# Kernel optimization log

Hardware: AMD Instinct MI355X
Metric: run time of the kernel (lower is better)

Reference implementation:

```python
import jax, jax.numpy as jnp
import numpy as np

B, S, D, H = 4, 2048, 2048, 16
DK = D // H  # 128
EPS = 1e-6


def setup_inputs() -> dict:
    key = jax.random.key(0)
    ks = jax.random.split(key, 8)
    scale = 1.0 / np.sqrt(D)
    return {
        "q": jax.random.normal(ks[0], (B, S, D), jnp.float32),
        "k": jax.random.normal(ks[1], (B, S, D), jnp.float32),
        "v": jax.random.normal(ks[2], (B, S, D), jnp.float32),
        "Wq": jax.random.normal(ks[3], (D, D), jnp.float32) * scale,
        "Wk": jax.random.normal(ks[4], (D, D), jnp.float32) * scale,
        "Wv": jax.random.normal(ks[5], (D, D), jnp.float32) * scale,
        "Wo": jax.random.normal(ks[6], (D, D), jnp.float32) * scale,
        "gamma": jnp.ones((D,), jnp.float32),
        "beta": jnp.zeros((D,), jnp.float32),
    }


def reference(q, k, v, Wq, Wk, Wv, Wo, gamma, beta):
    residual = q
    # projections (Linear with weight (out,in): x @ W^T)
    Q = (q @ Wq.T).reshape(B, S, H, DK)
    K = (k @ Wk.T).reshape(B, S, H, DK)
    V = (v @ Wv.T).reshape(B, S, H, DK)
    # faithful to source: permute(2,0,1,3) then flatten -> head-major (H*B, S, DK)
    Q = jnp.transpose(Q, (2, 0, 1, 3)).reshape(H * B, S, DK)
    K = jnp.transpose(K, (2, 0, 1, 3)).reshape(H * B, S, DK)
    V = jnp.transpose(V, (2, 0, 1, 3)).reshape(H * B, S, DK)
    scores = jnp.einsum("nqd,nkd->nqk", Q, K) / jnp.sqrt(jnp.float32(DK))
    attn = jax.nn.softmax(scores, axis=-1)  # (H*B, S, S)
    context = jnp.einsum("nqk,nkd->nqd", attn, V)
    # faithful to source: view (H*B,S,DK) as (B,H,S,DK) (batch-major reinterpretation)
    context = context.reshape(B, H, S, DK)
    context = jnp.transpose(context, (0, 2, 1, 3)).reshape(B, S, H * DK)
    output = context @ Wo.T  # dropout=0.0 (eval)
    output = output + residual
    mean = jnp.mean(output, axis=-1, keepdims=True)
    var = jnp.mean(jnp.square(output - mean), axis=-1, keepdims=True)
    output = (output - mean) / jnp.sqrt(var + EPS) * gamma + beta
    return output, attn
```

## Files before the change

kernel.cpp:

```cpp
#include <hip/hip_runtime.h>
#include <cstdint>

typedef __attribute__((ext_vector_type(8))) short short8;
typedef __attribute__((ext_vector_type(4))) float f32x4;
typedef __attribute__((ext_vector_type(2))) unsigned u32x2;
typedef unsigned short ushort_t;

constexpr int Bc = 4, Sc = 2048, Dc = 2048, Hc = 16, DKc = 128;
constexpr long NTOK = (long)Bc * Sc;
constexpr long OUT_ELEMS = NTOK * (long)Dc;
constexpr float SCALE = 0.08838834764831843f;

__device__ __forceinline__ ushort_t f2bf(float f) {
  unsigned u = __builtin_bit_cast(unsigned, f);
  u = (u + 0x7FFFu + ((u >> 16) & 1u)) >> 16;
  return (ushort_t)u;
}

__device__ __forceinline__ short8 pack8(const f32x4& a, const f32x4& b) {
  short8 h;
  h[0] = (short)f2bf(a[0]); h[1] = (short)f2bf(a[1]);
  h[2] = (short)f2bf(a[2]); h[3] = (short)f2bf(a[3]);
  h[4] = (short)f2bf(b[0]); h[5] = (short)f2bf(b[1]);
  h[6] = (short)f2bf(b[2]); h[7] = (short)f2bf(b[3]);
  return h;
}

__device__ __forceinline__ void gl2lds16(const ushort_t* g, ushort_t* l) {
  __builtin_amdgcn_global_load_lds(
      (__attribute__((address_space(1))) unsigned int*)(g),
      (__attribute__((address_space(3))) unsigned int*)(l), 16, 0, 0);
}

__device__ __forceinline__ void bar() {
  asm volatile("" ::: "memory");
  __builtin_amdgcn_s_barrier();
  asm volatile("" ::: "memory");
}

__global__ __launch_bounds__(512, 2)
void proj_gemm(const float* __restrict__ qf, const float* __restrict__ kf,
               const float* __restrict__ vf,
               const ushort_t* __restrict__ Wqb, const ushort_t* __restrict__ Wkb,
               const ushort_t* __restrict__ Wvb,
               ushort_t* __restrict__ Qb, ushort_t* __restrict__ Kb,
               ushort_t* __restrict__ VTo)
{
  __shared__ __align__(16) ushort_t SM[2][2][2][128 * 64];

  const int z = blockIdx.z;
  const float* Afull = (z == 0) ? qf : (z == 1) ? kf : vf;
  const ushort_t* Bp = (z == 0) ? Wqb : (z == 1) ? Wkb : Wvb;
  ushort_t* Cp = (z == 0) ? Qb : (z == 1) ? Kb : VTo;

  const int tid = threadIdx.x, lane = tid & 63, wave = tid >> 6;
  const int wm = wave >> 2, wn = wave & 3;

  const int lin = blockIdx.y * 8 + blockIdx.x;
  const int swz = (lin & 7) * 32 + (lin >> 3);
  const long n0 = (long)(swz & 7) * 256;
  const long m0 = (long)(swz >> 3) * 256;

  constexpr int NT = 32;

  const float*    Ag = Afull + m0 * (long)Dc;
  const ushort_t* Bg = Bp + n0 * (long)Dc;

  auto stageB = [&](ushort_t* dst, int kt, int ht) {
#pragma unroll
    for (int c = 0; c < 2; ++c) {
      int U = (c * 8 + wave) * 64 + lane;
      int row = U >> 3, p = U & 7, u = p ^ (row & 7);
      gl2lds16(Bg + (long)(ht * 128 + row) * Dc + kt * 64 + u * 8,
               dst + (c * 8 + wave) * 512);
    }
  };
  auto loadA = [&](int kt, f32x4 alo[2][2], f32x4 ahi[2][2]) {
#pragma unroll
    for (int ht = 0; ht < 2; ++ht)
#pragma unroll
      for (int c = 0; c < 2; ++c) {
        int U = (c * 8 + wave) * 64 + lane;
        int row = U >> 3, p = U & 7, u = p ^ (row & 7);
        const float* g = Ag + (long)(ht * 128 + row) * Dc + kt * 64 + u * 8;
        alo[ht][c] = *(const f32x4*)g;
        ahi[ht][c] = *(const f32x4*)(g + 4);
      }
  };
  auto writeA = [&](int buf, const f32x4 alo[2][2], const f32x4 ahi[2][2]) {
#pragma unroll
    for (int ht = 0; ht < 2; ++ht)
#pragma unroll
      for (int c = 0; c < 2; ++c) {
        int chunk = c * 8 + wave;
        *(short8*)(&SM[0][buf][ht][chunk * 512 + lane * 8]) =
            pack8(alo[ht][c], ahi[ht][c]);
      }
  };

  stageB(&SM[1][0][0][0], 0, 0);
  stageB(&SM[1][0][1][0], 0, 1);
  stageB(&SM[1][1][0][0], 1, 0);
  {
    f32x4 alo[2][2], ahi[2][2];
    loadA(0, alo, ahi);
    asm volatile("s_waitcnt vmcnt(0)" ::: "memory");
    writeA(0, alo, ahi);
    asm volatile("s_waitcnt lgkmcnt(0)" ::: "memory");
  }
  __builtin_amdgcn_s_barrier();
  asm volatile("" ::: "memory");

  f32x4 acc[8][4] = {};

  for (int kt = 0; kt < NT; ++kt) {
    const int cur = kt & 1;
    const ushort_t* Acur = &SM[0][cur][0][0];
    const ushort_t* Bcur = &SM[1][cur][0][0];
    const int k1 = (kt + 1) & (NT - 1);
    const int k2 = (kt + 2) & (NT - 1);
    short8 af[4][2], bq0[2][2], bq1[2][2];
    f32x4 alo[2][2], ahi[2][2];

#pragma unroll
    for (int mf = 0; mf < 4; ++mf)
#pragma unroll
      for (int ks = 0; ks < 2; ++ks) {
        int r = mf * 16 + (lane & 15);
        int u = ks * 4 + (lane >> 4), p = u ^ (r & 7);
        af[mf][ks] = *(const short8*)(Acur + wm * (128 * 64) + r * 64 + p * 8);
      }
#pragma unroll
    for (int nf = 0; nf < 2; ++nf)
#pragma unroll
      for (int ks = 0; ks < 2; ++ks) {
        int r = (wn & 1) * 64 + nf * 16 + (lane & 15);
        int u = ks * 4 + (lane >> 4), p = u ^ (r & 7);
        bq0[nf][ks] = *(const short8*)(Bcur + (wn >> 1) * (128 * 64) + r * 64 + p * 8);
      }
    stageB(&SM[1][cur ^ 1][1][0], k1, 1);
    bar();
    __builtin_amdgcn_s_setprio(1);
#pragma unroll
    for (int mf = 0; mf < 4; ++mf)
#pragma unroll
      for (int nf = 0; nf < 2; ++nf)
#pragma unroll
        for (int ks = 0; ks < 2; ++ks)
          acc[mf][nf] = __builtin_amdgcn_mfma_f32_16x16x32_bf16(af[mf][ks], bq0[nf][ks], acc[mf][nf], 0, 0, 0);
    __builtin_amdgcn_s_setprio(0);
    bar();

#pragma unroll
    for (int nf = 0; nf < 2; ++nf)
#pragma unroll
      for (int ks = 0; ks < 2; ++ks) {
        int r = (wn & 1) * 64 + 32 + nf * 16 + (lane & 15);
        int u = ks * 4 + (lane >> 4), p = u ^ (r & 7);
        bq1[nf][ks] = *(const short8*)(Bcur + (wn >> 1) * (128 * 64) + r * 64 + p * 8);
      }
    loadA(k1, alo, ahi);
    bar();
    __builtin_amdgcn_s_setprio(1);
#pragma unroll
    for (int mf = 0; mf < 4; ++mf)
#pragma unroll
      for (int nf = 0; nf < 2; ++nf)
#pragma unroll
        for (int ks = 0; ks < 2; ++ks)
          acc[mf][2 + nf] = __builtin_amdgcn_mfma_f32_16x16x32_bf16(af[mf][ks], bq1[nf][ks], acc[mf][2 + nf], 0, 0, 0);
    __builtin_amdgcn_s_setprio(0);
    bar();

#pragma unroll
    for (int mf = 0; mf < 4; ++mf)
#pragma unroll
      for (int ks = 0; ks < 2; ++ks) {
        int r = 64 + mf * 16 + (lane & 15);
        int u = ks * 4 + (lane >> 4), p = u ^ (r & 7);
        af[mf][ks] = *(const short8*)(Acur + wm * (128 * 64) + r * 64 + p * 8);
      }
    stageB(&SM[1][cur][0][0], k2, 0);
    bar();
    __builtin_amdgcn_s_setprio(1);
#pragma unroll
    for (int mf = 0; mf < 4; ++mf)
#pragma unroll
      for (int nf = 0; nf < 2; ++nf)
#pragma unroll
        for (int ks = 0; ks < 2; ++ks)
          acc[4 + mf][nf] = __builtin_amdgcn_mfma_f32_16x16x32_bf16(af[mf][ks], bq0[nf][ks], acc[4 + mf][nf], 0, 0, 0);
    __builtin_amdgcn_s_setprio(0);
    bar();

    asm volatile("s_waitcnt vmcnt(2)" ::: "memory");
    writeA(cur ^ 1, alo, ahi);
    asm volatile("s_waitcnt lgkmcnt(0)" ::: "memory");
    bar();
    __builtin_amdgcn_s_setprio(1);
#pragma unroll
    for (int mf = 0; mf < 4; ++mf)
#pragma unroll
      for (int nf = 0; nf < 2; ++nf)
#pragma unroll
        for (int ks = 0; ks < 2; ++ks)
          acc[4 + mf][2 + nf] = __builtin_amdgcn_mfma_f32_16x16x32_bf16(af[mf][ks], bq1[nf][ks], acc[4 + mf][2 + nf], 0, 0, 0);
    __builtin_amdgcn_s_setprio(0);
    bar();
  }

  asm volatile("s_waitcnt vmcnt(0)" ::: "memory");

  if (z == 2) {
    bar();
    char* Tb = (char*)&SM[0][0][0][0];
#pragma unroll
    for (int mq = 0; mq < 8; ++mq) {
#pragma unroll
      for (int nq = 0; nq < 4; ++nq) {
        int rg = wm * 128 + (mq >> 2) * 64 + (mq & 3) * 16 + ((lane >> 4) * 4);
        int cg = wn * 64 + (nq >> 1) * 32 + (nq & 1) * 16 + (lane & 15);
        u32x2 t;
        t[0] = (unsigned)f2bf(acc[mq][nq][0]) | ((unsigned)f2bf(acc[mq][nq][1]) << 16);
        t[1] = (unsigned)f2bf(acc[mq][nq][2]) | ((unsigned)f2bf(acc[mq][nq][3]) << 16);
        int off = cg * 512 + (((rg >> 3) ^ (cg & 31)) * 16) + (rg & 7) * 2;
        *(u32x2*)(Tb + off) = t;
      }
    }
    bar();
    const long bq = m0 >> 11;
    const long s0 = m0 & 2047;
#pragma unroll
    for (int i = 0; i < 16; ++i) {
      int row = i * 16 + (tid >> 5);
      int un  = tid & 31;
      int p = un ^ (row & 31);
      short8 val = *(const short8*)(Tb + row * 512 + p * 16);
      long cgg = n0 + row;
      long vtrow = ((cgg >> 7) * 4 + bq) * 128 + (cgg & 127);
      *(short8*)(&Cp[vtrow * (long)Sc + s0 + un * 8]) = val;
    }
  } else {
#pragma unroll
    for (int mq = 0; mq < 8; ++mq) {
#pragma unroll
      for (int nq = 0; nq < 4; ++nq) {
#pragma unroll
        for (int j = 0; j < 4; ++j) {
          long rg = m0 + wm * 128 + (mq >> 2) * 64 + (mq & 3) * 16 + ((lane >> 4) * 4) + j;
          long cg = n0 + wn * 64 + (nq >> 1) * 32 + (nq & 1) * 16 + (lane & 15);
          Cp[rg * (long)Dc + cg] = f2bf(acc[mq][nq][j]);
        }
      }
    }
  }
}

__global__ __launch_bounds__(512, 2)
void out_gemm(const ushort_t* __restrict__ Ap, const ushort_t* __restrict__ Bp,
              float* __restrict__ Cp, const float* __restrict__ residual)
{
  __shared__ __align__(16) ushort_t SM[2][2][2][128 * 64];

  const int tid = threadIdx.x, lane = tid & 63, wave = tid >> 6;
  const int wm = wave >> 2, wn = wave & 3;
  const int lin = blockIdx.y * 8 + blockIdx.x;
  const int swz = (lin & 7) * 32 + (lin >> 3);
  const long n0 = (long)(swz & 7) * 256;
  const long m0 = (long)(swz >> 3) * 256;
  constexpr int NT = 32;

  const ushort_t* Ag = Ap + m0 * (long)Dc;
  const ushort_t* Bg = Bp + n0 * (long)Dc;

  auto stage = [&](const ushort_t* gb, ushort_t* dst, int kt, int ht) {
#pragma unroll
    for (int c = 0; c < 2; ++c) {
      int U = (c * 8 + wave) * 64 + lane;
      int row = U >> 3, p = U & 7, u = p ^ (row & 7);
      gl2lds16(gb + (long)(ht * 128 + row) * Dc + kt * 64 + u * 8,
               dst + (c * 8 + wave) * 512);
    }
  };

  stage(Bg, &SM[1][0][0][0], 0, 0);
  stage(Ag, &SM[0][0][0][0], 0, 0);
  stage(Bg, &SM[1][0][1][0], 0, 1);
  stage(Ag, &SM[0][0][1][0], 0, 1);
  stage(Bg, &SM[1][1][0][0], 1, 0);
  stage(Ag, &SM[0][1][0][0], 1, 0);
  asm volatile("s_waitcnt vmcnt(4)" ::: "memory");
  __builtin_amdgcn_s_barrier();
  asm volatile("" ::: "memory");

  f32x4 acc[8][4] = {};

  for (int kt = 0; kt < NT; ++kt) {
    const int cur = kt & 1;
    const ushort_t* Acur = &SM[0][cur][0][0];
    const ushort_t* Bcur = &SM[1][cur][0][0];
    const int k1 = (kt + 1) & (NT - 1);
    const int k2 = (kt + 2) & (NT - 1);
    short8 af[4][2], bq0[2][2], bq1[2][2];

#pragma unroll
    for (int mf = 0; mf < 4; ++mf)
#pragma unroll
      for (int ks = 0; ks < 2; ++ks) {
        int r = mf * 16 + (lane & 15);
        int u = ks * 4 + (lane >> 4), p = u ^ (r & 7);
        af[mf][ks] = *(const short8*)(Acur + wm * (128 * 64) + r * 64 + p * 8);
      }
#pragma unroll
    for (int nf = 0; nf < 2; ++nf)
#pragma unroll
      for (int ks = 0; ks < 2; ++ks) {
        int r = (wn & 1) * 64 + nf * 16 + (lane & 15);
        int u = ks * 4 + (lane >> 4), p = u ^ (r & 7);
        bq0[nf][ks] = *(const short8*)(Bcur + (wn >> 1) * (128 * 64) + r * 64 + p * 8);
      }
    stage(Bg, &SM[1][cur ^ 1][1][0], k1, 1);
    bar();
    __builtin_amdgcn_s_setprio(1);
#pragma unroll
    for (int mf = 0; mf < 4; ++mf)
#pragma unroll
      for (int nf = 0; nf < 2; ++nf)
#pragma unroll
        for (int ks = 0; ks < 2; ++ks)
          acc[mf][nf] = __builtin_amdgcn_mfma_f32_16x16x32_bf16(af[mf][ks], bq0[nf][ks], acc[mf][nf], 0, 0, 0);
    __builtin_amdgcn_s_setprio(0);
    bar();

#pragma unroll
    for (int nf = 0; nf < 2; ++nf)
#pragma unroll
      for (int ks = 0; ks < 2; ++ks) {
        int r = (wn & 1) * 64 + 32 + nf * 16 + (lane & 15);
        int u = ks * 4 + (lane >> 4), p = u ^ (r & 7);
        bq1[nf][ks] = *(const short8*)(Bcur + (wn >> 1) * (128 * 64) + r * 64 + p * 8);
      }
    stage(Ag, &SM[0][cur ^ 1][1][0], k1, 1);
    bar();
    __builtin_amdgcn_s_setprio(1);
#pragma unroll
    for (int mf = 0; mf < 4; ++mf)
#pragma unroll
      for (int nf = 0; nf < 2; ++nf)
#pragma unroll
        for (int ks = 0; ks < 2; ++ks)
          acc[mf][2 + nf] = __builtin_amdgcn_mfma_f32_16x16x32_bf16(af[mf][ks], bq1[nf][ks], acc[mf][2 + nf], 0, 0, 0);
    __builtin_amdgcn_s_setprio(0);
    bar();

#pragma unroll
    for (int mf = 0; mf < 4; ++mf)
#pragma unroll
      for (int ks = 0; ks < 2; ++ks) {
        int r = 64 + mf * 16 + (lane & 15);
        int u = ks * 4 + (lane >> 4), p = u ^ (r & 7);
        af[mf][ks] = *(const short8*)(Acur + wm * (128 * 64) + r * 64 + p * 8);
      }
    stage(Bg, &SM[1][cur][0][0], k2, 0);
    bar();
    __builtin_amdgcn_s_setprio(1);
#pragma unroll
    for (int mf = 0; mf < 4; ++mf)
#pragma unroll
      for (int nf = 0; nf < 2; ++nf)
#pragma unroll
        for (int ks = 0; ks < 2; ++ks)
          acc[4 + mf][nf] = __builtin_amdgcn_mfma_f32_16x16x32_bf16(af[mf][ks], bq0[nf][ks], acc[4 + mf][nf], 0, 0, 0);
    __builtin_amdgcn_s_setprio(0);
    bar();

    stage(Ag, &SM[0][cur][0][0], k2, 0);
    asm volatile("s_waitcnt vmcnt(4)" ::: "memory");
    bar();
    __builtin_amdgcn_s_setprio(1);
#pragma unroll
    for (int mf = 0; mf < 4; ++mf)
#pragma unroll
      for (int nf = 0; nf < 2; ++nf)
#pragma unroll
        for (int ks = 0; ks < 2; ++ks)
          acc[4 + mf][2 + nf] = __builtin_amdgcn_mfma_f32_16x16x32_bf16(af[mf][ks], bq1[nf][ks], acc[4 + mf][2 + nf], 0, 0, 0);
    __builtin_amdgcn_s_setprio(0);
    bar();
  }

  asm volatile("s_waitcnt vmcnt(0)" ::: "memory");

#pragma unroll
  for (int mq = 0; mq < 8; ++mq) {
#pragma unroll
    for (int nq = 0; nq < 4; ++nq) {
#pragma unroll
      for (int j = 0; j < 4; ++j) {
        long rg = m0 + wm * 128 + (mq >> 2) * 64 + (mq & 3) * 16 + ((lane >> 4) * 4) + j;
        long cg = n0 + wn * 64 + (nq >> 1) * 32 + (nq & 1) * 16 + (lane & 15);
        Cp[rg * (long)Dc + cg] = acc[mq][nq][j] + residual[rg * (long)Dc + cg];
      }
    }
  }
}

__global__ __launch_bounds__(256, 2)
void flash_attn(const ushort_t* __restrict__ Qb, const ushort_t* __restrict__ Kb,
                const ushort_t* __restrict__ VT, float* __restrict__ attn,
                ushort_t* __restrict__ Cb)
{
  __shared__ __align__(16) ushort_t Qs[128 * 128];
  __shared__ __align__(16) ushort_t Ks[64 * 128];
  __shared__ __align__(16) ushort_t Vs[128 * 64];
  __shared__ __align__(16) ushort_t Ps[128 * 64];

  const int tid = threadIdx.x, lane = tid & 63, wave = tid >> 6;
  const int wr = wave >> 1, wc = wave & 1;

  const int bid = blockIdx.x;
  const int xcd = bid & 7, slot = bid >> 3;
  const int n = xcd * 8 + (slot >> 4);
  const long m0 = (long)(slot & 15) * 128;
  const int b = n & 3, h = n >> 2;

  const ushort_t* Qg = Qb + ((long)b * Sc) * Dc + (long)h * DKc;
  const ushort_t* Kg = Kb + ((long)b * Sc) * Dc + (long)h * DKc;
  const ushort_t* Vg = VT + (long)n * DKc * (long)Sc;
  float* Pg = attn + (long)n * Sc * (long)Sc;

#pragma unroll
  for (int c8 = 0; c8 < 8; ++c8) {
    int chunk = c8 * 4 + wave;
    int U = chunk * 64 + lane;
    int row = U >> 4, p = U & 15, u = p ^ (row & 15);
    gl2lds16(Qg + (m0 + row) * (long)Dc + u * 8, &Qs[chunk * 512]);
  }

  auto kaddr = [&](int t, int c4) -> const short8* {
    int chunk = c4 * 4 + wave;
    int U = chunk * 64 + lane;
    int row = U >> 4, p = U & 15, u = p ^ (row & 15);
    return (const short8*)(Kg + ((long)t * 64 + row) * (long)Dc + u * 8);
  };
  auto vaddr = [&](int t, int c4) -> const short8* {
    int chunk = c4 * 4 + wave;
    int U = chunk * 64 + lane;
    int row = U >> 3, p = U & 7, u = p ^ (row & 7);
    return (const short8*)(Vg + (long)row * Sc + (long)t * 64 + u * 8);
  };

  float rs[4][4] = {};

  short8 kr0 = *kaddr(0, 0), kr1 = *kaddr(0, 1), kr2_ = *kaddr(0, 2), kr3 = *kaddr(0, 3);
  for (int t = 0; t < 32; ++t) {
    __syncthreads();
    *(short8*)(&Ks[(0 * 4 + wave) * 512 + lane * 8]) = kr0;
    *(short8*)(&Ks[(1 * 4 + wave) * 512 + lane * 8]) = kr1;
    *(short8*)(&Ks[(2 * 4 + wave) * 512 + lane * 8]) = kr2_;
    *(short8*)(&Ks[(3 * 4 + wave) * 512 + lane * 8]) = kr3;
    __syncthreads();
    {
      int tn = (t + 1) & 31;
      kr0 = *kaddr(tn, 0); kr1 = *kaddr(tn, 1);
      kr2_ = *kaddr(tn, 2); kr3 = *kaddr(tn, 3);
    }
    f32x4 acc[4][2] = {};
#pragma unroll
    for (int kk = 0; kk < 4; ++kk) {
      short8 af[4], bfr[2];
#pragma unroll
      for (int m = 0; m < 4; ++m) {
        int row = wr * 64 + m * 16 + (lane & 15);
        int p = (kk * 4 + (lane >> 4)) ^ (row & 15);
        af[m] = *(const short8*)(&Qs[row * 128 + p * 8]);
      }
#pragma unroll
      for (int nn = 0; nn < 2; ++nn) {
        int row = wc * 32 + nn * 16 + (lane & 15);
        int p = (kk * 4 + (lane >> 4)) ^ (row & 15);
        bfr[nn] = *(const short8*)(&Ks[row * 128 + p * 8]);
      }
#pragma unroll
      for (int m = 0; m < 4; ++m)
#pragma unroll
        for (int nn = 0; nn < 2; ++nn)
          acc[m][nn] = __builtin_amdgcn_mfma_f32_16x16x32_bf16(af[m], bfr[nn], acc[m][nn], 0, 0, 0);
    }
#pragma unroll
    for (int m = 0; m < 4; ++m)
#pragma unroll
      for (int nn = 0; nn < 2; ++nn)
#pragma unroll
        for (int j = 0; j < 4; ++j)
          rs[m][j] += __expf(acc[m][nn][j] * SCALE);
  }

  short8 k0 = *kaddr(0, 0), k1_ = *kaddr(0, 1), k2_ = *kaddr(0, 2), k3 = *kaddr(0, 3);
  short8 v0 = *vaddr(0, 0), v1 = *vaddr(0, 1), v2 = *vaddr(0, 2), v3 = *vaddr(0, 3);

  float* red = (float*)Ps;
#pragma unroll
  for (int m = 0; m < 4; ++m)
#pragma unroll
    for (int j = 0; j < 4; ++j) {
#pragma unroll
      for (int off = 1; off < 16; off <<= 1)
        rs[m][j] += __shfl_xor(rs[m][j], off);
    }
  __syncthreads();
  if ((lane & 15) == 0) {
#pragma unroll
    for (int m = 0; m < 4; ++m)
#pragma unroll
      for (int j = 0; j < 4; ++j)
        red[wc * 128 + wr * 64 + m * 16 + ((lane >> 4) * 4) + j] = rs[m][j];
  }
  __syncthreads();
  float invl[4][4];
#pragma unroll
  for (int m = 0; m < 4; ++m)
#pragma unroll
    for (int j = 0; j < 4; ++j) {
      int row = wr * 64 + m * 16 + ((lane >> 4) * 4) + j;
      invl[m][j] = 1.f / (red[row] + red[128 + row]);
    }

  f32x4 acco[4][4] = {};
  for (int t = 0; t < 32; ++t) {
    __syncthreads();
    *(short8*)(&Ks[(0 * 4 + wave) * 512 + lane * 8]) = k0;
    *(short8*)(&Ks[(1 * 4 + wave) * 512 + lane * 8]) = k1_;
    *(short8*)(&Ks[(2 * 4 + wave) * 512 + lane * 8]) = k2_;
    *(short8*)(&Ks[(3 * 4 + wave) * 512 + lane * 8]) = k3;
    *(short8*)(&Vs[(0 * 4 + wave) * 512 + lane * 8]) = v0;
    *(short8*)(&Vs[(1 * 4 + wave) * 512 + lane * 8]) = v1;
    *(short8*)(&Vs[(2 * 4 + wave) * 512 + lane * 8]) = v2;
    *(short8*)(&Vs[(3 * 4 + wave) * 512 + lane * 8]) = v3;
    __syncthreads();
    {
      int tn = (t + 1) & 31;
      k0 = *kaddr(tn, 0); k1_ = *kaddr(tn, 1); k2_ = *kaddr(tn, 2); k3 = *kaddr(tn, 3);
      v0 = *vaddr(tn, 0); v1 = *vaddr(tn, 1); v2 = *vaddr(tn, 2); v3 = *vaddr(tn, 3);
    }
    f32x4 acc[4][2] = {};
#pragma unroll
    for (int kk = 0; kk < 4; ++kk) {
      short8 af[4], bfr[2];
#pragma unroll
      for (int m = 0; m < 4; ++m) {
        int row = wr * 64 + m * 16 + (lane & 15);
        int p = (kk * 4 + (lane >> 4)) ^ (row & 15);
        af[m] = *(const short8*)(&Qs[row * 128 + p * 8]);
      }
#pragma unroll
      for (int nn = 0; nn < 2; ++nn) {
        int row = wc * 32 + nn * 16 + (lane & 15);
        int p = (kk * 4 + (lane >> 4)) ^ (row & 15);
        bfr[nn] = *(const short8*)(&Ks[row * 128 + p * 8]);
      }
#pragma unroll
      for (int m = 0; m < 4; ++m)
#pragma unroll
        for (int nn = 0; nn < 2; ++nn)
          acc[m][nn] = __builtin_amdgcn_mfma_f32_16x16x32_bf16(af[m], bfr[nn], acc[m][nn], 0, 0, 0);
    }
#pragma unroll
    for (int m = 0; m < 4; ++m) {
#pragma unroll
      for (int nn = 0; nn < 2; ++nn) {
#pragma unroll
        for (int j = 0; j < 4; ++j) {
          float e = __expf(acc[m][nn][j] * SCALE) * invl[m][j];
          int row = wr * 64 + m * 16 + ((lane >> 4) * 4) + j;
          int col = wc * 32 + nn * 16 + (lane & 15);
          __builtin_nontemporal_store(e, &Pg[(m0 + row) * (long)Sc + (long)t * 64 + col]);
          int pp = (col >> 3) ^ (row & 7);
          Ps[row * 64 + pp * 8 + (col & 7)] = (ushort_t)f2bf(e);
        }
      }
    }
    __syncthreads();
#pragma unroll
    for (int ks = 0; ks < 2; ++ks) {
      short8 pa[4], vb[4];
#pragma unroll
      for (int m = 0; m < 4; ++m) {
        int row = wr * 64 + m * 16 + (lane & 15);
        int p = (ks * 4 + (lane >> 4)) ^ (row & 7);
        pa[m] = *(const short8*)(&Ps[row * 64 + p * 8]);
      }
#pragma unroll
      for (int nn = 0; nn < 4; ++nn) {
        int row = wc * 64 + nn * 16 + (lane & 15);
        int p = (ks * 4 + (lane >> 4)) ^ (row & 7);
        vb[nn] = *(const short8*)(&Vs[row * 64 + p * 8]);
      }
#pragma unroll
      for (int m = 0; m < 4; ++m)
#pragma unroll
        for (int nn = 0; nn < 4; ++nn)
          acco[m][nn] = __builtin_amdgcn_mfma_f32_16x16x32_bf16(pa[m], vb[nn], acco[m][nn], 0, 0, 0);
    }
  }

#pragma unroll
  for (int m = 0; m < 4; ++m) {
#pragma unroll
    for (int nn = 0; nn < 4; ++nn) {
#pragma unroll
      for (int j = 0; j < 4; ++j) {
        int row = wr * 64 + m * 16 + ((lane >> 4) * 4) + j;
        int col = wc * 64 + nn * 16 + (lane & 15);
        Cb[((long)(n >> 4) * Sc + m0 + row) * (long)Dc + (long)(n & 15) * DKc + col] =
            (ushort_t)f2bf(acco[m][nn][j]);
      }
    }
  }
}

__global__ __launch_bounds__(256)
void castW_bf16(const float* __restrict__ w0, const float* __restrict__ w1,
                const float* __restrict__ w2, const float* __restrict__ w3,
                ushort_t* __restrict__ o0, ushort_t* __restrict__ o1,
                ushort_t* __restrict__ o2, ushort_t* __restrict__ o3) {
  const float* in; ushort_t* out;
  switch (blockIdx.y) {
    case 0: in = w0; out = o0; break;
    case 1: in = w1; out = o1; break;
    case 2: in = w2; out = o2; break;
    default: in = w3; out = o3; break;
  }
  long i = ((long)blockIdx.x * 256 + threadIdx.x) * 8;
  f32x4 x = *(const f32x4*)(in + i);
  f32x4 y = *(const f32x4*)(in + i + 4);
  *(short8*)(out + i) = pack8(x, y);
}

__global__ __launch_bounds__(256)
void layernorm_rows(float* __restrict__ out, const float* __restrict__ gamma,
                    const float* __restrict__ beta) {
  const long row = blockIdx.x;
  float* p = out + row * (long)Dc;
  const int tid = threadIdx.x;
  const int lane = tid & 63, wave = tid >> 6;
  f32x4 v0 = *(const f32x4*)(p + tid * 8);
  f32x4 v1 = *(const f32x4*)(p + tid * 8 + 4);
  float s = 0.f, ss = 0.f;
#pragma unroll
  for (int e = 0; e < 4; ++e) { s += v0[e]; ss += v0[e] * v0[e]; }
#pragma unroll
  for (int e = 0; e < 4; ++e) { s += v1[e]; ss += v1[e] * v1[e]; }
  for (int off = 32; off > 0; off >>= 1) { s += __shfl_xor(s, off); ss += __shfl_xor(ss, off); }
  __shared__ float rs_[4], rss_[4];
  if (lane == 0) { rs_[wave] = s; rss_[wave] = ss; }
  __syncthreads();
  s  = rs_[0] + rs_[1] + rs_[2] + rs_[3];
  ss = rss_[0] + rss_[1] + rss_[2] + rss_[3];
  const float mean = s * (1.f / Dc);
  const float var  = ss * (1.f / Dc) - mean * mean;
  const float rstd = rsqrtf(var + 1e-6f);
  f32x4 g0 = *(const f32x4*)(gamma + tid * 8);
  f32x4 g1 = *(const f32x4*)(gamma + tid * 8 + 4);
  f32x4 b0 = *(const f32x4*)(beta + tid * 8);
  f32x4 b1 = *(const f32x4*)(beta + tid * 8 + 4);
#pragma unroll
  for (int e = 0; e < 4; ++e) v0[e] = (v0[e] - mean) * rstd * g0[e] + b0[e];
#pragma unroll
  for (int e = 0; e < 4; ++e) v1[e] = (v1[e] - mean) * rstd * g1[e] + b1[e];
  *(f32x4*)(p + tid * 8) = v0;
  *(f32x4*)(p + tid * 8 + 4) = v1;
}

extern "C" void kernel_launch(void* const* d_in, const int* in_sizes, int n_in,
                              void* d_out, int out_size, void* d_ws, size_t ws_size,
                              hipStream_t stream) {
  (void)in_sizes; (void)n_in; (void)out_size; (void)ws_size;
  const float* q  = (const float*)d_in[0];
  const float* k  = (const float*)d_in[1];
  const float* v  = (const float*)d_in[2];
  const float* Wq = (const float*)d_in[3];
  const float* Wk = (const float*)d_in[4];
  const float* Wv = (const float*)d_in[5];
  const float* Wo = (const float*)d_in[6];
  const float* gamma = (const float*)d_in[7];
  const float* beta  = (const float*)d_in[8];

  float* out  = (float*)d_out;
  float* attn = out + OUT_ELEMS;

  ushort_t* Wqb = (ushort_t*)d_ws;
  ushort_t* Wkb = Wqb + (long)Dc * Dc;
  ushort_t* Wvb = Wkb + (long)Dc * Dc;
  ushort_t* Wob = Wvb + (long)Dc * Dc;
  ushort_t* Qb  = Wob + (long)Dc * Dc;
  ushort_t* Kb  = Qb + OUT_ELEMS;
  ushort_t* VT  = Kb + OUT_ELEMS;
  ushort_t* Cb  = VT + OUT_ELEMS;

  castW_bf16<<<dim3((long)Dc * Dc / 2048, 4), dim3(256), 0, stream>>>(
      Wq, Wk, Wv, Wo, Wqb, Wkb, Wvb, Wob);

  proj_gemm<<<dim3(8, 32, 3), dim3(512), 0, stream>>>(
      q, k, v, Wqb, Wkb, Wvb, Qb, Kb, VT);

  flash_attn<<<dim3(1024), dim3(256), 0, stream>>>(Qb, Kb, VT, attn, Cb);

  out_gemm<<<dim3(8, 32), dim3(512), 0, stream>>>(Cb, Wob, out, q);

  layernorm_rows<<<NTOK, dim3(256), 0, stream>>>(out, gamma, beta);
}
```

Measured before the change: 749.1 us.

## Keep Q fragments in registers and alias LDS to shrink shared footprint

Loads the Q tile from LDS into per-wave register fragments once, then reuses that LDS region for K, V and P buffers, cutting shared memory from 80KB to 48KB. This removes the repeated Q LDS reads in every score loop and may allow more blocks per CU. It also moves the next-tile global K/V prefetch issue ahead of the barrier. The cost is 64 extra VGPRs per thread for qf, which risks spills or lower occupancy under launch_bounds(256,2).

```diff
diff --git a/kernel.cpp b/kernel.cpp
--- a/kernel.cpp
+++ b/kernel.cpp
@@ -410,10 +410,10 @@
                 const ushort_t* __restrict__ VT, float* __restrict__ attn,
                 ushort_t* __restrict__ Cb)
 {
-  __shared__ __align__(16) ushort_t Qs[128 * 128];
-  __shared__ __align__(16) ushort_t Ks[64 * 128];
-  __shared__ __align__(16) ushort_t Vs[128 * 64];
-  __shared__ __align__(16) ushort_t Ps[128 * 64];
+  __shared__ __align__(16) ushort_t LDS[24576];
+  ushort_t* Ks = LDS;
+  ushort_t* Vs = LDS + 8192;
+  ushort_t* Ps = LDS + 16384;
 
   const int tid = threadIdx.x, lane = tid & 63, wave = tid >> 6;
   const int wr = wave >> 1, wc = wave & 1;
@@ -434,8 +434,20 @@
     int chunk = c8 * 4 + wave;
     int U = chunk * 64 + lane;
     int row = U >> 4, p = U & 15, u = p ^ (row & 15);
-    gl2lds16(Qg + (m0 + row) * (long)Dc + u * 8, &Qs[chunk * 512]);
-  }
+    gl2lds16(Qg + (m0 + row) * (long)Dc + u * 8, &LDS[chunk * 512]);
+  }
+  asm volatile("s_waitcnt vmcnt(0)" ::: "memory");
+  __syncthreads();
+  short8 qf[4][4];
+#pragma unroll
+  for (int m = 0; m < 4; ++m)
+#pragma unroll
+    for (int kk = 0; kk < 4; ++kk) {
+      int row = wr * 64 + m * 16 + (lane & 15);
+      int p = (kk * 4 + (lane >> 4)) ^ (row & 15);
+      qf[m][kk] = *(const short8*)(&LDS[row * 128 + p * 8]);
+    }
+  __syncthreads();
 
   auto kaddr = [&](int t, int c4) -> const short8* {
     int chunk = c4 * 4 + wave;
@@ -459,22 +471,16 @@
     *(short8*)(&Ks[(1 * 4 + wave) * 512 + lane * 8]) = kr1;
     *(short8*)(&Ks[(2 * 4 + wave) * 512 + lane * 8]) = kr2_;
     *(short8*)(&Ks[(3 * 4 + wave) * 512 + lane * 8]) = kr3;
-    __syncthreads();
     {
       int tn = (t + 1) & 31;
       kr0 = *kaddr(tn, 0); kr1 = *kaddr(tn, 1);
       kr2_ = *kaddr(tn, 2); kr3 = *kaddr(tn, 3);
     }
+    __syncthreads();
     f32x4 acc[4][2] = {};
 #pragma unroll
     for (int kk = 0; kk < 4; ++kk) {
-      short8 af[4], bfr[2];
-#pragma unroll
-      for (int m = 0; m < 4; ++m) {
-        int row = wr * 64 + m * 16 + (lane & 15);
-        int p = (kk * 4 + (lane >> 4)) ^ (row & 15);
-        af[m] = *(const short8*)(&Qs[row * 128 + p * 8]);
-      }
+      short8 bfr[2];
 #pragma unroll
       for (int nn = 0; nn < 2; ++nn) {
         int row = wc * 32 + nn * 16 + (lane & 15);
@@ -485,7 +491,7 @@
       for (int m = 0; m < 4; ++m)
 #pragma unroll
         for (int nn = 0; nn < 2; ++nn)
-          acc[m][nn] = __builtin_amdgcn_mfma_f32_16x16x32_bf16(af[m], bfr[nn], acc[m][nn], 0, 0, 0);
+          acc[m][nn] = __builtin_amdgcn_mfma_f32_16x16x32_bf16(qf[m][kk], bfr[nn], acc[m][nn], 0, 0, 0);
     }
 #pragma unroll
     for (int m = 0; m < 4; ++m)
@@ -537,22 +543,16 @@
     *(short8*)(&Vs[(1 * 4 + wave) * 512 + lane * 8]) = v1;
     *(short8*)(&Vs[(2 * 4 + wave) * 512 + lane * 8]) = v2;
     *(short8*)(&Vs[(3 * 4 + wave) * 512 + lane * 8]) = v3;
-    __syncthreads();
     {
       int tn = (t + 1) & 31;
       k0 = *kaddr(tn, 0); k1_ = *kaddr(tn, 1); k2_ = *kaddr(tn, 2); k3 = *kaddr(tn, 3);
       v0 = *vaddr(tn, 0); v1 = *vaddr(tn, 1); v2 = *vaddr(tn, 2); v3 = *vaddr(tn, 3);
     }
+    __syncthreads();
     f32x4 acc[4][2] = {};
 #pragma unroll
     for (int kk = 0; kk < 4; ++kk) {
-      short8 af[4], bfr[2];
-#pragma unroll
-      for (int m = 0; m < 4; ++m) {
-        int row = wr * 64 + m * 16 + (lane & 15);
-        int p = (kk * 4 + (lane >> 4)) ^ (row & 15);
-        af[m] = *(const short8*)(&Qs[row * 128 + p * 8]);
-      }
+      short8 bfr[2];
 #pragma unroll
       for (int nn = 0; nn < 2; ++nn) {
         int row = wc * 32 + nn * 16 + (lane & 15);
@@ -563,7 +563,7 @@
       for (int m = 0; m < 4; ++m)
 #pragma unroll
         for (int nn = 0; nn < 2; ++nn)
-          acc[m][nn] = __builtin_amdgcn_mfma_f32_16x16x32_bf16(af[m], bfr[nn], acc[m][nn], 0, 0, 0);
+          acc[m][nn] = __builtin_amdgcn_mfma_f32_16x16x32_bf16(qf[m][kk], bfr[nn], acc[m][nn], 0, 0, 0);
     }
 #pragma unroll
     for (int m = 0; m < 4; ++m) {
```

New measurement: 993.2 us. 32.6% more time.

## Load K and V MFMA fragments directly from global memory, dropping LDS staging

Applied to the files above, without the earlier changes.

The attention kernel stops staging K and V tiles through shared memory. Each wave now loads its MFMA B-operand fragments straight from global memory into registers, which removes the LDS stores and the barriers around them in both passes and shrinks the shared-memory footprint. In exchange, the two column-half waves that share K/V data each issue their own global loads, and the loads sit right before use without explicit double buffering, so latency may be exposed. It also adds an explicit vmcnt wait and barrier after the Q prefetch.

```diff
diff --git a/kernel.cpp b/kernel.cpp
--- a/kernel.cpp
+++ b/kernel.cpp
@@ -410,10 +410,9 @@
                 const ushort_t* __restrict__ VT, float* __restrict__ attn,
                 ushort_t* __restrict__ Cb)
 {
-  __shared__ __align__(16) ushort_t Qs[128 * 128];
-  __shared__ __align__(16) ushort_t Ks[64 * 128];
-  __shared__ __align__(16) ushort_t Vs[128 * 64];
-  __shared__ __align__(16) ushort_t Ps[128 * 64];
+  __shared__ __align__(16) ushort_t LDS[24576];
+  ushort_t* Qs = LDS;
+  ushort_t* Ps = LDS + 16384;
 
   const int tid = threadIdx.x, lane = tid & 63, wave = tid >> 6;
   const int wr = wave >> 1, wc = wave & 1;
@@ -436,39 +435,31 @@
     int row = U >> 4, p = U & 15, u = p ^ (row & 15);
     gl2lds16(Qg + (m0 + row) * (long)Dc + u * 8, &Qs[chunk * 512]);
   }
-
-  auto kaddr = [&](int t, int c4) -> const short8* {
-    int chunk = c4 * 4 + wave;
-    int U = chunk * 64 + lane;
-    int row = U >> 4, p = U & 15, u = p ^ (row & 15);
-    return (const short8*)(Kg + ((long)t * 64 + row) * (long)Dc + u * 8);
+  asm volatile("s_waitcnt vmcnt(0)" ::: "memory");
+  __syncthreads();
+
+  auto kdirect = [&](int t, int kk, int nn) -> short8 {
+    int row = wc * 32 + nn * 16 + (lane & 15);
+    return *(const short8*)(Kg + ((long)t * 64 + row) * (long)Dc + (kk * 4 + (lane >> 4)) * 8);
   };
-  auto vaddr = [&](int t, int c4) -> const short8* {
-    int chunk = c4 * 4 + wave;
-    int U = chunk * 64 + lane;
-    int row = U >> 3, p = U & 7, u = p ^ (row & 7);
-    return (const short8*)(Vg + (long)row * Sc + (long)t * 64 + u * 8);
+  auto vdirect = [&](int t, int ks, int nn) -> short8 {
+    int row = wc * 64 + nn * 16 + (lane & 15);
+    return *(const short8*)(Vg + (long)row * Sc + (long)t * 64 + (ks * 4 + (lane >> 4)) * 8);
   };
 
   float rs[4][4] = {};
 
-  short8 kr0 = *kaddr(0, 0), kr1 = *kaddr(0, 1), kr2_ = *kaddr(0, 2), kr3 = *kaddr(0, 3);
   for (int t = 0; t < 32; ++t) {
-    __syncthreads();
-    *(short8*)(&Ks[(0 * 4 + wave) * 512 + lane * 8]) = kr0;
-    *(short8*)(&Ks[(1 * 4 + wave) * 512 + lane * 8]) = kr1;
-    *(short8*)(&Ks[(2 * 4 + wave) * 512 + lane * 8]) = kr2_;
-    *(short8*)(&Ks[(3 * 4 + wave) * 512 + lane * 8]) = kr3;
-    __syncthreads();
-    {
-      int tn = (t + 1) & 31;
-      kr0 = *kaddr(tn, 0); kr1 = *kaddr(tn, 1);
-      kr2_ = *kaddr(tn, 2); kr3 = *kaddr(tn, 3);
-    }
+    short8 bfr[4][2];
+#pragma unroll
+    for (int kk = 0; kk < 4; ++kk)
+#pragma unroll
+      for (int nn = 0; nn < 2; ++nn)
+        bfr[kk][nn] = kdirect(t, kk, nn);
     f32x4 acc[4][2] = {};
 #pragma unroll
     for (int kk = 0; kk < 4; ++kk) {
-      short8 af[4], bfr[2];
+      short8 af[4];
 #pragma unroll
       for (int m = 0; m < 4; ++m) {
         int row = wr * 64 + m * 16 + (lane & 15);
@@ -476,16 +467,10 @@
         af[m] = *(const short8*)(&Qs[row * 128 + p * 8]);
       }
 #pragma unroll
-      for (int nn = 0; nn < 2; ++nn) {
-        int row = wc * 32 + nn * 16 + (lane & 15);
-        int p = (kk * 4 + (lane >> 4)) ^ (row & 15);
-        bfr[nn] = *(const short8*)(&Ks[row * 128 + p * 8]);
-      }
-#pragma unroll
       for (int m = 0; m < 4; ++m)
 #pragma unroll
         for (int nn = 0; nn < 2; ++nn)
-          acc[m][nn] = __builtin_amdgcn_mfma_f32_16x16x32_bf16(af[m], bfr[nn], acc[m][nn], 0, 0, 0);
+          acc[m][nn] = __builtin_amdgcn_mfma_f32_16x16x32_bf16(af[m], bfr[kk][nn], acc[m][nn], 0, 0, 0);
     }
 #pragma unroll
     for (int m = 0; m < 4; ++m)
@@ -496,9 +481,6 @@
           rs[m][j] += __expf(acc[m][nn][j] * SCALE);
   }
 
-  short8 k0 = *kaddr(0, 0), k1_ = *kaddr(0, 1), k2_ = *kaddr(0, 2), k3 = *kaddr(0, 3);
-  short8 v0 = *vaddr(0, 0), v1 = *vaddr(0, 1), v2 = *vaddr(0, 2), v3 = *vaddr(0, 3);
-
   float* red = (float*)Ps;
 #pragma unroll
   for (int m = 0; m < 4; ++m)
@@ -508,7 +490,6 @@
       for (int off = 1; off < 16; off <<= 1)
         rs[m][j] += __shfl_xor(rs[m][j], off);
     }
-  __syncthreads();
   if ((lane & 15) == 0) {
 #pragma unroll
     for (int m = 0; m < 4; ++m)
@@ -529,24 +510,21 @@
   f32x4 acco[4][4] = {};
   for (int t = 0; t < 32; ++t) {
     __syncthreads();
-    *(short8*)(&Ks[(0 * 4 + wave) * 512 + lane * 8]) = k0;
-    *(short8*)(&Ks[(1 * 4 + wave) * 512 + lane * 8]) = k1_;
-    *(short8*)(&Ks[(2 * 4 + wave) * 512 + lane * 8]) = k2_;
-    *(short8*)(&Ks[(3 * 4 + wave) * 512 + lane * 8]) = k3;
-    *(short8*)(&Vs[(0 * 4 + wave) * 512 + lane * 8]) = v0;
-    *(short8*)(&Vs[(1 * 4 + wave) * 512 + lane * 8]) = v1;
-    *(short8*)(&Vs[(2 * 4 + wave) * 512 + lane * 8]) = v2;
-    *(short8*)(&Vs[(3 * 4 + wave) * 512 + lane * 8]) = v3;
-    __syncthreads();
-    {
-      int tn = (t + 1) & 31;
-      k0 = *kaddr(tn, 0); k1_ = *kaddr(tn, 1); k2_ = *kaddr(tn, 2); k3 = *kaddr(tn, 3);
-      v0 = *vaddr(tn, 0); v1 = *vaddr(tn, 1); v2 = *vaddr(tn, 2); v3 = *vaddr(tn, 3);
-    }
+    short8 bfr[4][2], vb[2][4];
+#pragma unroll
+    for (int kk = 0; kk < 4; ++kk)
+#pragma unroll
+      for (int nn = 0; nn < 2; ++nn)
+        bfr[kk][nn] = kdirect(t, kk, nn);
+#pragma unroll
+    for (int ks = 0; ks < 2; ++ks)
+#pragma unroll
+      for (int nn = 0; nn < 4; ++nn)
+        vb[ks][nn] = vdirect(t, ks, nn);
     f32x4 acc[4][2] = {};
 #pragma unroll
     for (int kk = 0; kk < 4; ++kk) {
-      short8 af[4], bfr[2];
+      short8 af[4];
 #pragma unroll
       for (int m = 0; m < 4; ++m) {
         int row = wr * 64 + m * 16 + (lane & 15);
@@ -554,16 +532,10 @@
         af[m] = *(const short8*)(&Qs[row * 128 + p * 8]);
       }
 #pragma unroll
-      for (int nn = 0; nn < 2; ++nn) {
-        int row = wc * 32 + nn * 16 + (lane & 15);
-        int p = (kk * 4 + (lane >> 4)) ^ (row & 15);
-        bfr[nn] = *(const short8*)(&Ks[row * 128 + p * 8]);
-      }
-#pragma unroll
       for (int m = 0; m < 4; ++m)
 #pragma unroll
         for (int nn = 0; nn < 2; ++nn)
-          acc[m][nn] = __builtin_amdgcn_mfma_f32_16x16x32_bf16(af[m], bfr[nn], acc[m][nn], 0, 0, 0);
+          acc[m][nn] = __builtin_amdgcn_mfma_f32_16x16x32_bf16(af[m], bfr[kk][nn], acc[m][nn], 0, 0, 0);
     }
 #pragma unroll
     for (int m = 0; m < 4; ++m) {
@@ -583,7 +555,7 @@
     __syncthreads();
 #pragma unroll
     for (int ks = 0; ks < 2; ++ks) {
-      short8 pa[4], vb[4];
+      short8 pa[4];
 #pragma unroll
       for (int m = 0; m < 4; ++m) {
         int row = wr * 64 + m * 16 + (lane & 15);
@@ -591,16 +563,10 @@
         pa[m] = *(const short8*)(&Ps[row * 64 + p * 8]);
       }
 #pragma unroll
-      for (int nn = 0; nn < 4; ++nn) {
-        int row = wc * 64 + nn * 16 + (lane & 15);
-        int p = (ks * 4 + (lane >> 4)) ^ (row & 7);
-        vb[nn] = *(const short8*)(&Vs[row * 64 + p * 8]);
-      }
-#pragma unroll
       for (int m = 0; m < 4; ++m)
 #pragma unroll
         for (int nn = 0; nn < 4; ++nn)
-          acco[m][nn] = __builtin_amdgcn_mfma_f32_16x16x32_bf16(pa[m], vb[nn], acco[m][nn], 0, 0, 0);
+          acco[m][nn] = __builtin_amdgcn_mfma_f32_16x16x32_bf16(pa[m], vb[ks][nn], acco[m][nn], 0, 0, 0);
     }
   }
 
```

After: 818.2 us. 1.09x slower.
